# Kernel tuning notes

Hardware: AMD Instinct MI355X
Metric: run time of the kernel (lower is better)

Reference implementation:

```python
import jax, jax.numpy as jnp
import numpy as np

B, T, D, H = 2, 2048, 1024, 16
HD = D // H  # head_dim = 64


def setup_inputs() -> dict:
    key = jax.random.key(0)
    ks = jax.random.split(key, 5)
    s = 0.02
    return {
        "x": jax.random.normal(ks[0], (B, T, D), dtype=jnp.float32),
        "Wqkv": jax.random.normal(ks[1], (3 * D, D), dtype=jnp.float32) * s,
        "bqkv": jax.random.normal(ks[2], (3 * D,), dtype=jnp.float32) * s,
        "Wproj": jax.random.normal(ks[3], (D, D), dtype=jnp.float32) * s,
        "bproj": jax.random.normal(ks[4], (D,), dtype=jnp.float32) * s,
    }


def reference(x, Wqkv, bqkv, Wproj, bproj):
    b, t, d = x.shape
    qkv = x @ Wqkv.T + bqkv                      # [B,T,3D]
    q, k, v = jnp.split(qkv, 3, axis=-1)
    # [B,T,D] -> [B,H,T,HD]
    def to_heads(u):
        return u.reshape(b, t, H, HD).transpose(0, 2, 1, 3)
    q, k, v = to_heads(q), to_heads(k), to_heads(v)
    scale = 1.0 / jnp.sqrt(jnp.float32(HD))
    attn = jnp.einsum("bhqd,bhkd->bhqk", q, k) * scale   # [B,H,T,T]
    causal = jnp.tril(jnp.ones((t, t), dtype=bool))
    attn = jnp.where(causal[None, None, :, :], attn, -jnp.inf)
    attn = jax.nn.softmax(attn, axis=-1)
    scores = jnp.einsum("bhqk,bhkd->bhqd", attn, v)       # [B,H,T,HD]
    scores = scores.transpose(0, 2, 1, 3).reshape(b, t, d)
    return scores @ Wproj.T + bproj
```

## Files before the change

### kernel.cpp

```cpp
#include <hip/hip_runtime.h>

typedef __bf16 bf16_8 __attribute__((ext_vector_type(8)));
typedef __bf16 bf16_4 __attribute__((ext_vector_type(4)));
typedef float  f32_4  __attribute__((ext_vector_type(4)));

typedef __attribute__((address_space(1))) const void* as1_cvp;
typedef __attribute__((address_space(3))) void*       as3_vp;

__device__ __forceinline__ void load16_to_lds(const void* g, void* l) {
    __builtin_amdgcn_global_load_lds((as1_cvp)g, (as3_vp)l, 16, 0, 0);
}

__global__ __launch_bounds__(256) void cvt_all(
    const float* __restrict__ a, const float* __restrict__ b,
    const float* __restrict__ c, __bf16* __restrict__ out,
    int na4, int nb4, int nc4)
{
    int i = blockIdx.x * 256 + threadIdx.x;
    if (i >= na4 + nb4 + nc4) return;
    float4 f;
    if (i < na4)            f = ((const float4*)a)[i];
    else if (i < na4 + nb4) f = ((const float4*)b)[i - na4];
    else                    f = ((const float4*)c)[i - na4 - nb4];
    bf16_4 v = { (__bf16)f.x, (__bf16)f.y, (__bf16)f.z, (__bf16)f.w };
    ((bf16_4*)out)[i] = v;
}

#define BM 128

template<int OUT_BF16, int BN_>
__global__ __launch_bounds__(256) void gemm_bt(
    const __bf16* __restrict__ A,
    const __bf16* __restrict__ B,
    const float*  __restrict__ bias,
    __bf16* __restrict__ Cb, float* __restrict__ Cf,
    int M, int N, int K)
{
    constexpr int NT   = BN_ / 32;
    constexpr int CSTR = BN_ + (OUT_BF16 ? 8 : 4);
    __shared__ __align__(16) char smem[35840];
    __bf16* As = (__bf16*)smem;
    __bf16* Bs = As + 128 * 64;

    const int tid  = threadIdx.x;
    const int wave = tid >> 6;
    const int lane = tid & 63;
    const int wm = wave >> 1, wn = wave & 1;
    const int quad = lane >> 4, l16 = lane & 15;
    const int bm = blockIdx.y * BM, bn = blockIdx.x * BN_;

    const int r0 = tid >> 3;
    const int ch = tid & 7;
    const int cs = (ch ^ (r0 & 7)) * 8;

    f32_4 acc[4][NT];
    #pragma unroll
    for (int i = 0; i < 4; ++i)
        #pragma unroll
        for (int j = 0; j < NT; ++j)
            acc[i][j] = f32_4{0.f, 0.f, 0.f, 0.f};

    for (int k0 = 0; k0 < K; k0 += 64) {
        __syncthreads();
        #pragma unroll
        for (int p = 0; p < 4; ++p) {
            int row = p * 32 + r0;
            load16_to_lds(A + (size_t)(bm + row) * K + k0 + cs,
                          &As[(p * 32 + wave * 8) * 64]);
        }
        #pragma unroll
        for (int p = 0; p < BN_ / 32; ++p) {
            int row = p * 32 + r0;
            load16_to_lds(B + (size_t)(bn + row) * K + k0 + cs,
                          &Bs[(p * 32 + wave * 8) * 64]);
        }
        __syncthreads();

        #pragma unroll
        for (int h = 0; h < 2; ++h) {
            const int sl = ((quad + h * 4) ^ (l16 & 7)) * 8;
            bf16_8 af[4], bfr[NT];
            #pragma unroll
            for (int mt = 0; mt < 4; ++mt)
                af[mt] = *(const bf16_8*)&As[(wm * 64 + mt * 16 + l16) * 64 + sl];
            #pragma unroll
            for (int nt = 0; nt < NT; ++nt)
                bfr[nt] = *(const bf16_8*)&Bs[(wn * (BN_/2) + nt * 16 + l16) * 64 + sl];
            #pragma unroll
            for (int mt = 0; mt < 4; ++mt)
                #pragma unroll
                for (int nt = 0; nt < NT; ++nt)
                    acc[mt][nt] = __builtin_amdgcn_mfma_f32_16x16x32_bf16(
                        af[mt], bfr[nt], acc[mt][nt], 0, 0, 0);
        }
    }

    __syncthreads();

    if (OUT_BF16) {
        __bf16* Cs = (__bf16*)smem;
        #pragma unroll
        for (int mt = 0; mt < 4; ++mt)
            #pragma unroll
            for (int nt = 0; nt < NT; ++nt) {
                int col = wn * (BN_/2) + nt * 16 + l16;
                float bv = bias ? bias[bn + col] : 0.f;
                #pragma unroll
                for (int r = 0; r < 4; ++r)
                    Cs[(wm * 64 + mt * 16 + quad * 4 + r) * CSTR + col] =
                        (__bf16)(acc[mt][nt][r] + bv);
            }
        __syncthreads();
        const int rr = tid >> 4, cc = (tid & 15) * 8;
        #pragma unroll
        for (int p = 0; p < 8; ++p) {
            int row = p * 16 + rr;
            bf16_8 v = *(const bf16_8*)&Cs[row * CSTR + cc];
            *(bf16_8*)(Cb + (size_t)(bm + row) * N + bn + cc) = v;
        }
    } else {
        float* Cs = (float*)smem;
        #pragma unroll
        for (int mt = 0; mt < 4; ++mt)
            #pragma unroll
            for (int nt = 0; nt < NT; ++nt) {
                int col = wn * (BN_/2) + nt * 16 + l16;
                float bv = bias ? bias[bn + col] : 0.f;
                #pragma unroll
                for (int r = 0; r < 4; ++r)
                    Cs[(wm * 64 + mt * 16 + quad * 4 + r) * CSTR + col] =
                        acc[mt][nt][r] + bv;
            }
        __syncthreads();
        const int rr = tid >> 4, cc = (tid & 15) * 4;
        #pragma unroll
        for (int p = 0; p < 8; ++p) {
            int row = p * 16 + rr;
            float4 v = *(const float4*)&Cs[row * CSTR + cc];
            *(float4*)(Cf + (size_t)(bm + row) * N + bn + cc) = v;
        }
    }
}

__global__ __launch_bounds__(512) void attn_kernel(
    const __bf16* __restrict__ qkv, __bf16* __restrict__ out)
{
    constexpr int T = 2048;
    __shared__ __align__(16) char pool[53760];
    __bf16* Ks = (__bf16*)pool;
    __bf16* Vt = (__bf16*)(pool + 16384);
    __bf16* Ps = (__bf16*)(pool + 32768);
    float*  Lm = (float*)(pool + 53248);
    float*  Om = (float*)pool;

    const int tid  = threadIdx.x;
    const int wave = tid >> 6;
    const int lane = tid & 63;
    const int wg = wave >> 2, wq = wave & 3;
    const int quad = lane >> 4, l16 = lane & 15;

    const int fid = blockIdx.x;
    const int xcd = fid & 7;
    const int loc = fid >> 3;
    const int bh  = xcd * 4 + (loc >> 3);
    const int z   = loc & 7;
    const int b = bh >> 4, h = bh & 15;

    const size_t rowbase = (size_t)b * T;
    const __bf16* Kbase = qkv + 1024 + h * 64;
    const __bf16* Vbase = qkv + 2048 + h * 64;

    const int krow = tid >> 3;
    const int kcbs = tid & 7;
    const int kcbf = kcbs ^ (krow & 7);
    const int vrow = krow, va = kcbs;

    #pragma unroll
    for (int tile = 0; tile < 2; ++tile) {
        const int qt = tile ? (15 - z) : z;
        const int jmax = 2 * qt + 1;

        bf16_8 aq[2][2];
        #pragma unroll
        for (int mt = 0; mt < 2; ++mt) {
            const __bf16* qrow =
                qkv + (rowbase + qt * 128 + wq * 32 + mt * 16 + l16) * 3072 + h * 64;
            aq[mt][0] = *(const bf16_8*)(qrow + quad * 8);
            aq[mt][1] = *(const bf16_8*)(qrow + 32 + quad * 8);
            #pragma unroll
            for (int u = 0; u < 8; ++u) {
                aq[mt][0][u] = (__bf16)((float)aq[mt][0][u] * 0.125f);
                aq[mt][1][u] = (__bf16)((float)aq[mt][1][u] * 0.125f);
            }
        }

        load16_to_lds(Kbase + (rowbase + krow) * 3072 + kcbf * 8, &Ks[wave * 512]);
        {
            bf16_8 vv = *(const bf16_8*)(Vbase + (rowbase + vrow) * 3072 + va * 8);
            int kc = vrow >> 3, kl = vrow & 7;
            #pragma unroll
            for (int u = 0; u < 8; ++u)
                Vt[(va * 8 + u) * 64 + ((kc ^ u ^ va) << 3) + kl] = vv[u];
        }

        float l_i[2][4];
        f32_4 O[2][4];
        #pragma unroll
        for (int mt = 0; mt < 2; ++mt) {
            #pragma unroll
            for (int r = 0; r < 4; ++r) l_i[mt][r] = 0.f;
            #pragma unroll
            for (int dt = 0; dt < 4; ++dt) O[mt][dt] = f32_4{0.f, 0.f, 0.f, 0.f};
        }

        for (int j = 0; j <= jmax; ++j) {
            const int cur = j & 1, nxt = cur ^ 1;
            __syncthreads();

            const bool stage = (j < jmax);
            bf16_8 vv;
            if (stage) {
                const int jn = j + 1;
                load16_to_lds(Kbase + (rowbase + jn * 64 + krow) * 3072 + kcbf * 8,
                              &Ks[nxt * 4096 + wave * 512]);
                vv = *(const bf16_8*)(Vbase + (rowbase + jn * 64 + vrow) * 3072 + va * 8);
            }

            f32_4 S[2][2];
            #pragma unroll
            for (int nt = 0; nt < 2; ++nt) {
                int rk = wg * 32 + nt * 16 + l16;
                int rx = rk & 7;
                bf16_8 kb0 = *(const bf16_8*)&Ks[cur * 4096 + rk * 64 + ((quad ^ rx) << 3)];
                bf16_8 kb1 = *(const bf16_8*)&Ks[cur * 4096 + rk * 64 + (((quad + 4) ^ rx) << 3)];
                #pragma unroll
                for (int mt = 0; mt < 2; ++mt) {
                    f32_4 zz = {0.f, 0.f, 0.f, 0.f};
                    zz = __builtin_amdgcn_mfma_f32_16x16x32_bf16(aq[mt][0], kb0, zz, 0, 0, 0);
                    zz = __builtin_amdgcn_mfma_f32_16x16x32_bf16(aq[mt][1], kb1, zz, 0, 0, 0);
                    S[mt][nt] = zz;
                }
            }

            const bool diag = (j >= 2 * qt);
            #pragma unroll
            for (int mt = 0; mt < 2; ++mt)
                #pragma unroll
                for (int r = 0; r < 4; ++r) {
                    float p0 = __expf(S[mt][0][r]);
                    float p1 = __expf(S[mt][1][r]);
                    if (diag) {
                        int qg = qt * 128 + wq * 32 + mt * 16 + quad * 4 + r;
                        if (j * 64 + wg * 32 + l16      > qg) p0 = 0.f;
                        if (j * 64 + wg * 32 + 16 + l16 > qg) p1 = 0.f;
                    }
                    l_i[mt][r] += p0 + p1;
                    int prow = mt * 16 + quad * 4 + r;
                    Ps[wave * 1280 + prow * 40 + l16]      = (__bf16)p0;
                    Ps[wave * 1280 + prow * 40 + 16 + l16] = (__bf16)p1;
                }

            bf16_8 ap[2];
            #pragma unroll
            for (int mt = 0; mt < 2; ++mt)
                ap[mt] = *(const bf16_8*)&Ps[wave * 1280 + (mt * 16 + l16) * 40 + quad * 8];
            #pragma unroll
            for (int dt = 0; dt < 4; ++dt) {
                int d = dt * 16 + l16;
                int cb = (wg * 4 + quad) ^ (d & 7) ^ ((d >> 3) & 7);
                bf16_8 vb = *(const bf16_8*)&Vt[cur * 4096 + d * 64 + (cb << 3)];
                #pragma unroll
                for (int mt = 0; mt < 2; ++mt)
                    O[mt][dt] = __builtin_amdgcn_mfma_f32_16x16x32_bf16(ap[mt], vb, O[mt][dt], 0, 0, 0);
            }

            if (stage) {
                int kc = vrow >> 3, kl = vrow & 7;
                #pragma unroll
                for (int u = 0; u < 8; ++u)
                    Vt[nxt * 4096 + (va * 8 + u) * 64 + ((kc ^ u ^ va) << 3) + kl] = vv[u];
            }
        }

        float lrow[2][4];
        #pragma unroll
        for (int mt = 0; mt < 2; ++mt)
            #pragma unroll
            for (int r = 0; r < 4; ++r) {
                float v = l_i[mt][r];
                #pragma unroll
                for (int off = 1; off <= 8; off <<= 1)
                    v += __shfl_xor(v, off, 64);
                lrow[mt][r] = v;
            }
        __syncthreads();
        if (wg == 1) {
            #pragma unroll
            for (int mt = 0; mt < 2; ++mt)
                #pragma unroll
                for (int r = 0; r < 4; ++r) {
                    int row = mt * 16 + quad * 4 + r;
                    #pragma unroll
                    for (int dt = 0; dt < 4; ++dt)
                        Om[wq * 2176 + row * 68 + dt * 16 + l16] = O[mt][dt][r];
                    if (l16 == 0) Lm[wq * 32 + row] = lrow[mt][r];
                }
        }
        __syncthreads();
        if (wg == 0) {
            #pragma unroll
            for (int mt = 0; mt < 2; ++mt)
                #pragma unroll
                for (int r = 0; r < 4; ++r) {
                    int row = mt * 16 + quad * 4 + r;
                    float inv = 1.f / (lrow[mt][r] + Lm[wq * 32 + row]);
                    int q = qt * 128 + wq * 32 + row;
                    #pragma unroll
                    for (int dt = 0; dt < 4; ++dt) {
                        float val = (O[mt][dt][r] + Om[wq * 2176 + row * 68 + dt * 16 + l16]) * inv;
                        out[(rowbase + q) * 1024 + h * 64 + dt * 16 + l16] = (__bf16)val;
                    }
                }
        }
        __syncthreads();
    }
}

extern "C" void kernel_launch(void* const* d_in, const int* in_sizes, int n_in,
                              void* d_out, int out_size, void* d_ws, size_t ws_size,
                              hipStream_t stream)
{
    constexpr int Bc = 2, Tc = 2048, Dc = 1024;
    constexpr int M  = Bc * Tc;
    constexpr int N1 = 3 * Dc;

    const float* x     = (const float*)d_in[0];
    const float* Wqkv  = (const float*)d_in[1];
    const float* bqkv  = (const float*)d_in[2];
    const float* Wproj = (const float*)d_in[3];
    const float* bproj = (const float*)d_in[4];
    float* outp = (float*)d_out;

    __bf16* xb     = (__bf16*)d_ws;
    __bf16* wqkvb  = xb     + (size_t)M * Dc;
    __bf16* wprojb = wqkvb  + (size_t)N1 * Dc;
    __bf16* qkvb   = wprojb + (size_t)Dc * Dc;
    __bf16* attnb  = qkvb   + (size_t)M * N1;

    {
        int na4 = M * Dc / 4, nb4 = N1 * Dc / 4, nc4 = Dc * Dc / 4;
        int n4 = na4 + nb4 + nc4;
        cvt_all<<<(n4 + 255) / 256, 256, 0, stream>>>(x, Wqkv, Wproj, xb, na4, nb4, nc4);
    }

    gemm_bt<1, 128><<<dim3(N1 / 128, M / BM), 256, 0, stream>>>(
        xb, wqkvb, bqkv, qkvb, nullptr, M, N1, Dc);

    attn_kernel<<<dim3(256), 512, 0, stream>>>(qkvb, attnb);

    gemm_bt<0, 64><<<dim3(Dc / 64, M / BM), 256, 0, stream>>>(
        attnb, wprojb, bproj, nullptr, outp, M, Dc, Dc);
}
```

Baseline: 178.7 us.

## Keep attention probabilities in registers via transposed MFMA, one q-tile per block

Computes S transposed (K as the A operand) so each lane's exp'd probabilities line up as a 16x16x16 MFMA B operand. P is fed straight from registers into the PV product, which removes the per-iteration LDS round trip through the Ps buffer. With that buffer gone, the shared pool shrinks and launch bounds request 4 blocks per CU. The grid doubles to one q-tile per block, ordered longest-first, replacing the paired short/long tiles per block. The risks are uneven tail work, since blocks now differ in length, and the extra MFMA instructions of the smaller 16x16x16 shape in the PV step.

```diff
diff --git a/kernel.cpp b/kernel.cpp
--- a/kernel.cpp
+++ b/kernel.cpp
@@ -3,12 +3,22 @@
 typedef __bf16 bf16_8 __attribute__((ext_vector_type(8)));
 typedef __bf16 bf16_4 __attribute__((ext_vector_type(4)));
 typedef float  f32_4  __attribute__((ext_vector_type(4)));
+typedef short  s16x4  __attribute__((ext_vector_type(4)));
 
 typedef __attribute__((address_space(1))) const void* as1_cvp;
 typedef __attribute__((address_space(3))) void*       as3_vp;
 
 __device__ __forceinline__ void load16_to_lds(const void* g, void* l) {
     __builtin_amdgcn_global_load_lds((as1_cvp)g, (as3_vp)l, 16, 0, 0);
+}
+
+__device__ __forceinline__ f32_4 mfma16x16x16(bf16_4 a, bf16_4 b, f32_4 c) {
+#if __has_builtin(__builtin_amdgcn_mfma_f32_16x16x16_bf16)
+    return __builtin_amdgcn_mfma_f32_16x16x16_bf16(a, b, c, 0, 0, 0);
+#else
+    return __builtin_amdgcn_mfma_f32_16x16x16bf16_1k(
+        __builtin_bit_cast(s16x4, a), __builtin_bit_cast(s16x4, b), c, 0, 0, 0);
+#endif
 }
 
 __global__ __launch_bounds__(256) void cvt_all(
@@ -142,16 +152,15 @@
     }
 }
 
-__global__ __launch_bounds__(512) void attn_kernel(
+__global__ __launch_bounds__(512, 4) void attn_kernel(
     const __bf16* __restrict__ qkv, __bf16* __restrict__ out)
 {
     constexpr int T = 2048;
-    __shared__ __align__(16) char pool[53760];
+    __shared__ __align__(16) char pool[35328];
     __bf16* Ks = (__bf16*)pool;
     __bf16* Vt = (__bf16*)(pool + 16384);
-    __bf16* Ps = (__bf16*)(pool + 32768);
-    float*  Lm = (float*)(pool + 53248);
     float*  Om = (float*)pool;
+    float*  Lm = (float*)(pool + 34816);
 
     const int tid  = threadIdx.x;
     const int wave = tid >> 6;
@@ -161,10 +170,11 @@
 
     const int fid = blockIdx.x;
     const int xcd = fid & 7;
-    const int loc = fid >> 3;
-    const int bh  = xcd * 4 + (loc >> 3);
-    const int z   = loc & 7;
+    const int w   = fid >> 3;
+    const int qt  = 15 - (w >> 2);
+    const int bh  = xcd * 4 + (w & 3);
     const int b = bh >> 4, h = bh & 15;
+    const int jmax = 2 * qt + 1;
 
     const size_t rowbase = (size_t)b * T;
     const __bf16* Kbase = qkv + 1024 + h * 64;
@@ -175,154 +185,142 @@
     const int kcbf = kcbs ^ (krow & 7);
     const int vrow = krow, va = kcbs;
 
+    bf16_8 aq[2][2];
     #pragma unroll
-    for (int tile = 0; tile < 2; ++tile) {
-        const int qt = tile ? (15 - z) : z;
-        const int jmax = 2 * qt + 1;
-
-        bf16_8 aq[2][2];
+    for (int mt = 0; mt < 2; ++mt) {
+        const __bf16* qrow =
+            qkv + (rowbase + qt * 128 + wq * 32 + mt * 16 + l16) * 3072 + h * 64;
+        aq[mt][0] = *(const bf16_8*)(qrow + quad * 8);
+        aq[mt][1] = *(const bf16_8*)(qrow + 32 + quad * 8);
+        #pragma unroll
+        for (int u = 0; u < 8; ++u) {
+            aq[mt][0][u] = (__bf16)((float)aq[mt][0][u] * 0.125f);
+            aq[mt][1][u] = (__bf16)((float)aq[mt][1][u] * 0.125f);
+        }
+    }
+
+    load16_to_lds(Kbase + (rowbase + krow) * 3072 + kcbf * 8, &Ks[wave * 512]);
+    {
+        bf16_8 vv = *(const bf16_8*)(Vbase + (rowbase + vrow) * 3072 + va * 8);
+        int kc = vrow >> 3, kl = vrow & 7;
+        #pragma unroll
+        for (int u = 0; u < 8; ++u)
+            Vt[(va * 8 + u) * 64 + ((kc ^ u ^ va) << 3) + kl] = vv[u];
+    }
+
+    float l_i[2] = {0.f, 0.f};
+    f32_4 O[2][4];
+    #pragma unroll
+    for (int mt = 0; mt < 2; ++mt)
+        #pragma unroll
+        for (int dt = 0; dt < 4; ++dt) O[mt][dt] = f32_4{0.f, 0.f, 0.f, 0.f};
+
+    for (int j = 0; j <= jmax; ++j) {
+        const int cur = j & 1, nxt = cur ^ 1;
+        __syncthreads();
+
+        const bool stage = (j < jmax);
+        bf16_8 vv;
+        if (stage) {
+            const int jn = j + 1;
+            load16_to_lds(Kbase + (rowbase + jn * 64 + krow) * 3072 + kcbf * 8,
+                          &Ks[nxt * 4096 + wave * 512]);
+            vv = *(const bf16_8*)(Vbase + (rowbase + jn * 64 + vrow) * 3072 + va * 8);
+        }
+
+        f32_4 S[2][2];
+        #pragma unroll
+        for (int nt = 0; nt < 2; ++nt) {
+            int rk = wg * 32 + nt * 16 + l16;
+            int rx = rk & 7;
+            bf16_8 kb0 = *(const bf16_8*)&Ks[cur * 4096 + rk * 64 + ((quad ^ rx) << 3)];
+            bf16_8 kb1 = *(const bf16_8*)&Ks[cur * 4096 + rk * 64 + (((quad + 4) ^ rx) << 3)];
+            #pragma unroll
+            for (int mt = 0; mt < 2; ++mt) {
+                f32_4 zz = {0.f, 0.f, 0.f, 0.f};
+                zz = __builtin_amdgcn_mfma_f32_16x16x32_bf16(kb0, aq[mt][0], zz, 0, 0, 0);
+                zz = __builtin_amdgcn_mfma_f32_16x16x32_bf16(kb1, aq[mt][1], zz, 0, 0, 0);
+                S[mt][nt] = zz;
+            }
+        }
+
+        const bool diag = (j >= 2 * qt);
+        bf16_4 bp[2][2];
         #pragma unroll
         for (int mt = 0; mt < 2; ++mt) {
-            const __bf16* qrow =
-                qkv + (rowbase + qt * 128 + wq * 32 + mt * 16 + l16) * 3072 + h * 64;
-            aq[mt][0] = *(const bf16_8*)(qrow + quad * 8);
-            aq[mt][1] = *(const bf16_8*)(qrow + 32 + quad * 8);
-            #pragma unroll
-            for (int u = 0; u < 8; ++u) {
-                aq[mt][0][u] = (__bf16)((float)aq[mt][0][u] * 0.125f);
-                aq[mt][1][u] = (__bf16)((float)aq[mt][1][u] * 0.125f);
-            }
-        }
-
-        load16_to_lds(Kbase + (rowbase + krow) * 3072 + kcbf * 8, &Ks[wave * 512]);
-        {
-            bf16_8 vv = *(const bf16_8*)(Vbase + (rowbase + vrow) * 3072 + va * 8);
+            int qg = qt * 128 + wq * 32 + mt * 16 + l16;
+            #pragma unroll
+            for (int nt = 0; nt < 2; ++nt) {
+                #pragma unroll
+                for (int rr = 0; rr < 4; ++rr) {
+                    float p = __expf(S[mt][nt][rr]);
+                    if (diag) {
+                        int key = j * 64 + wg * 32 + nt * 16 + quad * 4 + rr;
+                        if (key > qg) p = 0.f;
+                    }
+                    l_i[mt] += p;
+                    bp[mt][nt][rr] = (__bf16)p;
+                }
+            }
+        }
+
+        #pragma unroll
+        for (int dt = 0; dt < 4; ++dt) {
+            int d = dt * 16 + l16;
+            int dsw = (d & 7) ^ ((d >> 3) & 7);
+            #pragma unroll
+            for (int nt = 0; nt < 2; ++nt) {
+                int kc16 = wg * 2 + nt;
+                int chv = (kc16 * 2 + (quad >> 1)) ^ dsw;
+                bf16_4 vaf = *(const bf16_4*)&Vt[cur * 4096 + d * 64 + chv * 8 + (quad & 1) * 4];
+                #pragma unroll
+                for (int mt = 0; mt < 2; ++mt)
+                    O[mt][dt] = mfma16x16x16(vaf, bp[mt][nt], O[mt][dt]);
+            }
+        }
+
+        if (stage) {
             int kc = vrow >> 3, kl = vrow & 7;
             #pragma unroll
             for (int u = 0; u < 8; ++u)
-                Vt[(va * 8 + u) * 64 + ((kc ^ u ^ va) << 3) + kl] = vv[u];
-        }
-
-        float l_i[2][4];
-        f32_4 O[2][4];
+                Vt[nxt * 4096 + (va * 8 + u) * 64 + ((kc ^ u ^ va) << 3) + kl] = vv[u];
+        }
+    }
+
+    float lw[2];
+    #pragma unroll
+    for (int mt = 0; mt < 2; ++mt) {
+        float v = l_i[mt];
+        v += __shfl_xor(v, 16, 64);
+        v += __shfl_xor(v, 32, 64);
+        lw[mt] = v;
+    }
+    __syncthreads();
+    if (wg == 1) {
         #pragma unroll
         for (int mt = 0; mt < 2; ++mt) {
             #pragma unroll
-            for (int r = 0; r < 4; ++r) l_i[mt][r] = 0.f;
-            #pragma unroll
-            for (int dt = 0; dt < 4; ++dt) O[mt][dt] = f32_4{0.f, 0.f, 0.f, 0.f};
-        }
-
-        for (int j = 0; j <= jmax; ++j) {
-            const int cur = j & 1, nxt = cur ^ 1;
-            __syncthreads();
-
-            const bool stage = (j < jmax);
-            bf16_8 vv;
-            if (stage) {
-                const int jn = j + 1;
-                load16_to_lds(Kbase + (rowbase + jn * 64 + krow) * 3072 + kcbf * 8,
-                              &Ks[nxt * 4096 + wave * 512]);
-                vv = *(const bf16_8*)(Vbase + (rowbase + jn * 64 + vrow) * 3072 + va * 8);
-            }
-
-            f32_4 S[2][2];
-            #pragma unroll
-            for (int nt = 0; nt < 2; ++nt) {
-                int rk = wg * 32 + nt * 16 + l16;
-                int rx = rk & 7;
-                bf16_8 kb0 = *(const bf16_8*)&Ks[cur * 4096 + rk * 64 + ((quad ^ rx) << 3)];
-                bf16_8 kb1 = *(const bf16_8*)&Ks[cur * 4096 + rk * 64 + (((quad + 4) ^ rx) << 3)];
-                #pragma unroll
-                for (int mt = 0; mt < 2; ++mt) {
-                    f32_4 zz = {0.f, 0.f, 0.f, 0.f};
-                    zz = __builtin_amdgcn_mfma_f32_16x16x32_bf16(aq[mt][0], kb0, zz, 0, 0, 0);
-                    zz = __builtin_amdgcn_mfma_f32_16x16x32_bf16(aq[mt][1], kb1, zz, 0, 0, 0);
-                    S[mt][nt] = zz;
-                }
-            }
-
-            const bool diag = (j >= 2 * qt);
-            #pragma unroll
-            for (int mt = 0; mt < 2; ++mt)
-                #pragma unroll
-                for (int r = 0; r < 4; ++r) {
-                    float p0 = __expf(S[mt][0][r]);
-                    float p1 = __expf(S[mt][1][r]);
-                    if (diag) {
-                        int qg = qt * 128 + wq * 32 + mt * 16 + quad * 4 + r;
-                        if (j * 64 + wg * 32 + l16      > qg) p0 = 0.f;
-                        if (j * 64 + wg * 32 + 16 + l16 > qg) p1 = 0.f;
-                    }
-                    l_i[mt][r] += p0 + p1;
-                    int prow = mt * 16 + quad * 4 + r;
-                    Ps[wave * 1280 + prow * 40 + l16]      = (__bf16)p0;
-                    Ps[wave * 1280 + prow * 40 + 16 + l16] = (__bf16)p1;
-                }
-
-            bf16_8 ap[2];
-            #pragma unroll
-            for (int mt = 0; mt < 2; ++mt)
-                ap[mt] = *(const bf16_8*)&Ps[wave * 1280 + (mt * 16 + l16) * 40 + quad * 8];
+            for (int dt = 0; dt < 4; ++dt)
+                *(f32_4*)&Om[(wq * 32 + mt * 16 + l16) * 68 + dt * 16 + quad * 4] = O[mt][dt];
+            if (quad == 0) Lm[wq * 32 + mt * 16 + l16] = lw[mt];
+        }
+    }
+    __syncthreads();
+    if (wg == 0) {
+        #pragma unroll
+        for (int mt = 0; mt < 2; ++mt) {
+            float inv = 1.f / (lw[mt] + Lm[wq * 32 + mt * 16 + l16]);
+            int q = qt * 128 + wq * 32 + mt * 16 + l16;
             #pragma unroll
             for (int dt = 0; dt < 4; ++dt) {
-                int d = dt * 16 + l16;
-                int cb = (wg * 4 + quad) ^ (d & 7) ^ ((d >> 3) & 7);
-                bf16_8 vb = *(const bf16_8*)&Vt[cur * 4096 + d * 64 + (cb << 3)];
-                #pragma unroll
-                for (int mt = 0; mt < 2; ++mt)
-                    O[mt][dt] = __builtin_amdgcn_mfma_f32_16x16x32_bf16(ap[mt], vb, O[mt][dt], 0, 0, 0);
-            }
-
-            if (stage) {
-                int kc = vrow >> 3, kl = vrow & 7;
-                #pragma unroll
-                for (int u = 0; u < 8; ++u)
-                    Vt[nxt * 4096 + (va * 8 + u) * 64 + ((kc ^ u ^ va) << 3) + kl] = vv[u];
-            }
-        }
-
-        float lrow[2][4];
-        #pragma unroll
-        for (int mt = 0; mt < 2; ++mt)
-            #pragma unroll
-            for (int r = 0; r < 4; ++r) {
-                float v = l_i[mt][r];
-                #pragma unroll
-                for (int off = 1; off <= 8; off <<= 1)
-                    v += __shfl_xor(v, off, 64);
-                lrow[mt][r] = v;
-            }
-        __syncthreads();
-        if (wg == 1) {
-            #pragma unroll
-            for (int mt = 0; mt < 2; ++mt)
-                #pragma unroll
-                for (int r = 0; r < 4; ++r) {
-                    int row = mt * 16 + quad * 4 + r;
-                    #pragma unroll
-                    for (int dt = 0; dt < 4; ++dt)
-                        Om[wq * 2176 + row * 68 + dt * 16 + l16] = O[mt][dt][r];
-                    if (l16 == 0) Lm[wq * 32 + row] = lrow[mt][r];
-                }
-        }
-        __syncthreads();
-        if (wg == 0) {
-            #pragma unroll
-            for (int mt = 0; mt < 2; ++mt)
-                #pragma unroll
-                for (int r = 0; r < 4; ++r) {
-                    int row = mt * 16 + quad * 4 + r;
-                    float inv = 1.f / (lrow[mt][r] + Lm[wq * 32 + row]);
-                    int q = qt * 128 + wq * 32 + row;
-                    #pragma unroll
-                    for (int dt = 0; dt < 4; ++dt) {
-                        float val = (O[mt][dt][r] + Om[wq * 2176 + row * 68 + dt * 16 + l16]) * inv;
-                        out[(rowbase + q) * 1024 + h * 64 + dt * 16 + l16] = (__bf16)val;
-                    }
-                }
-        }
-        __syncthreads();
+                f32_4 o2 = *(const f32_4*)&Om[(wq * 32 + mt * 16 + l16) * 68 + dt * 16 + quad * 4];
+                bf16_4 ov;
+                #pragma unroll
+                for (int rr = 0; rr < 4; ++rr)
+                    ov[rr] = (__bf16)((O[mt][dt][rr] + o2[rr]) * inv);
+                *(bf16_4*)(out + (rowbase + q) * 1024 + h * 64 + dt * 16 + quad * 4) = ov;
+            }
+        }
     }
 }
 
@@ -356,7 +354,7 @@
     gemm_bt<1, 128><<<dim3(N1 / 128, M / BM), 256, 0, stream>>>(
         xb, wqkvb, bqkv, qkvb, nullptr, M, N1, Dc);
 
-    attn_kernel<<<dim3(256), 512, 0, stream>>>(qkvb, attnb);
+    attn_kernel<<<dim3(512), 512, 0, stream>>>(qkvb, attnb);
 
     gemm_bt<0, 64><<<dim3(Dc / 64, M / BM), 256, 0, stream>>>(
         attnb, wprojb, bproj, nullptr, outp, M, Dc, Dc);
```

Measured after the change: 179.3 us. About the same (+0.3%).
